# Kernel tuning notes

Hardware: AMD Instinct MI355X
Metric: run time of the kernel (lower is better)

## Reference

```python
import jax, jax.numpy as jnp
import numpy as np

D_IN = 1024
D_OUT = 1024
N_HEADS = 16
HEAD_DIM = D_OUT // N_HEADS


def setup_inputs() -> dict:
    key = jax.random.key(0)
    ks = jax.random.split(key, 5)
    scale = 0.02
    x = jax.random.normal(ks[0], (2, 2048, D_IN), dtype=jnp.float32)
    Wq = jax.random.normal(ks[1], (D_IN, D_OUT), dtype=jnp.float32) * scale
    Wk = jax.random.normal(ks[2], (D_IN, D_OUT), dtype=jnp.float32) * scale
    Wv = jax.random.normal(ks[3], (D_IN, D_OUT), dtype=jnp.float32) * scale
    Wout = jax.random.normal(ks[4], (D_OUT, D_OUT), dtype=jnp.float32) * scale
    return {"x": x, "Wq": Wq, "Wk": Wk, "Wv": Wv, "Wout": Wout}


def reference(x, Wq, Wk, Wv, Wout):
    batch, seq_len, _ = x.shape
    # projections (no bias)
    Q = (x @ Wq).reshape(batch, seq_len, N_HEADS, HEAD_DIM)
    K = (x @ Wk).reshape(batch, seq_len, N_HEADS, HEAD_DIM)
    V = (x @ Wv).reshape(batch, seq_len, N_HEADS, HEAD_DIM)
    # scores: [batch, heads, seq, seq]
    scores = jnp.einsum("bqhd,bkhd->bhqk", Q, K) / jnp.sqrt(
        jnp.asarray(HEAD_DIM, dtype=x.dtype)
    )
    # causal mask: positions k > q masked to -inf
    causal = jnp.tril(jnp.ones((seq_len, seq_len), dtype=bool))
    scores = jnp.where(causal[None, None], scores, -jnp.inf)
    weights = jax.nn.softmax(scores, axis=-1)
    vectors = jnp.einsum("bhqk,bkhd->bqhd", weights, V)
    vectors = vectors.reshape(batch, seq_len, D_OUT)
    return vectors @ Wout
```

## Files before the change

### kernel.cpp

```cpp
#include <hip/hip_runtime.h>
#include <hip/hip_bf16.h>


typedef __attribute__((ext_vector_type(8))) _Float16 vhalf8;
typedef __attribute__((ext_vector_type(4))) _Float16 vhalf4;
typedef __attribute__((ext_vector_type(4))) float vfloat4;

#define D_MODEL 1024
#define SEQ     2048
#define NB      2
#define NH      16
#define HD      64

#define SCALE_K1 0.18033688f

__device__ __forceinline__ void async16(const void* g, void* l) {
  __builtin_amdgcn_global_load_lds(
      (const __attribute__((address_space(1))) unsigned int*)g,
      (__attribute__((address_space(3))) unsigned int*)l, 16, 0, 0);
}

__global__ __launch_bounds__(256) void cvt_f32_f16(
    const float* __restrict__ in, _Float16* __restrict__ out) {
  size_t i = ((size_t)blockIdx.x * 256 + threadIdx.x) * 8;
  float4 a = *(const float4*)&in[i];
  float4 b = *(const float4*)&in[i + 4];
  vhalf8 h;
  h[0] = (_Float16)a.x; h[1] = (_Float16)a.y;
  h[2] = (_Float16)a.z; h[3] = (_Float16)a.w;
  h[4] = (_Float16)b.x; h[5] = (_Float16)b.y;
  h[6] = (_Float16)b.z; h[7] = (_Float16)b.w;
  *(vhalf8*)&out[i] = h;
}

__global__ __launch_bounds__(256) void transpose_w4(
    const float* __restrict__ Wq, const float* __restrict__ Wk,
    const float* __restrict__ Wv, const float* __restrict__ Wo,
    _Float16* __restrict__ Wt_qkv, _Float16* __restrict__ Wot) {
  __shared__ _Float16 tile[64][65];
  int z = blockIdx.z;
  const float* in = (z == 0) ? Wq : (z == 1) ? Wk : (z == 2) ? Wv : Wo;
  _Float16* out = (z < 3) ? (Wt_qkv + (size_t)z * 1024 * 1024) : Wot;
  int c0 = blockIdx.x * 64, r0 = blockIdx.y * 64;
  int t = threadIdx.x;
  int tc = t & 63, tr = t >> 6;
#pragma unroll
  for (int p = 0; p < 16; p++) {
    int r = tr + p * 4;
    tile[r][tc] = (_Float16)in[(size_t)(r0 + r) * 1024 + c0 + tc];
  }
  __syncthreads();
#pragma unroll
  for (int p = 0; p < 16; p++) {
    int r = tr + p * 4;
    out[(size_t)(c0 + r) * 1024 + r0 + tc] = tile[tc][r];
  }
}

__global__ __launch_bounds__(256) void gemm128(
    const _Float16* __restrict__ A, const _Float16* __restrict__ Bt,
    _Float16* __restrict__ Ch, float* __restrict__ Cf,
    _Float16* __restrict__ Vt, int M, int N, int K, int mode) {
  __shared__ _Float16 As[128 * 32];
  __shared__ _Float16 Bs[128 * 32];
  int m0 = blockIdx.x * 128, n0 = blockIdx.y * 128;
  int t = threadIdx.x;
  int lane = t & 63, wave = t >> 6;
  int wm = (wave >> 1) * 64, wn = (wave & 1) * 64;
  int col = lane & 15, quad = lane >> 4;
  int srow = lane >> 2;
  int skc = (lane & 3) << 3;

  vfloat4 acc[4][4];
#pragma unroll
  for (int i = 0; i < 4; i++)
#pragma unroll
    for (int j = 0; j < 4; j++) {
      acc[i][j][0] = 0.f; acc[i][j][1] = 0.f;
      acc[i][j][2] = 0.f; acc[i][j][3] = 0.f;
    }

  for (int k0 = 0; k0 < K; k0 += 32) {
    __syncthreads();
#pragma unroll
    for (int j = 0; j < 4; j++) {
      int c = wave * 4 + j;
      int row = ((c & 7) << 4) + srow;
      if (c < 8)
        async16(&A[(size_t)(m0 + row) * K + k0 + skc], &As[c * 512]);
      else
        async16(&Bt[(size_t)(n0 + row) * K + k0 + skc], &Bs[(c - 8) * 512]);
    }
    __syncthreads();

    vhalf8 af[4], bf[4];
#pragma unroll
    for (int i = 0; i < 4; i++) {
      af[i] = *(const vhalf8*)&As[(wm + i * 16 + col) * 32 + quad * 8];
      bf[i] = *(const vhalf8*)&Bs[(wn + i * 16 + col) * 32 + quad * 8];
    }
#pragma unroll
    for (int i = 0; i < 4; i++)
#pragma unroll
      for (int j = 0; j < 4; j++)
        acc[i][j] = __builtin_amdgcn_mfma_f32_16x16x32_f16(af[i], bf[j], acc[i][j], 0, 0, 0);
  }

  bool vmode = (mode == 2) && (n0 >= 2048);
#pragma unroll
  for (int i = 0; i < 4; i++)
#pragma unroll
    for (int j = 0; j < 4; j++)
#pragma unroll
      for (int r = 0; r < 4; r++) {
        int m = m0 + wm + i * 16 + quad * 4 + r;
        int n = n0 + wn + j * 16 + col;
        if (mode == 1) {
          Cf[(size_t)m * N + n] = acc[i][j][r];
        } else if (vmode) {
          int nn = n - 2048;
          int hh = nn >> 6, dd = nn & 63;
          int bb = m >> 11, ss = m & 2047;
          Vt[(((size_t)bb * NH + hh) * HD + dd) * SEQ + ss] = (_Float16)acc[i][j][r];
        } else {
          Ch[(size_t)m * N + n] = (_Float16)acc[i][j][r];
        }
      }
}

__global__ __launch_bounds__(256) void attn(
    const _Float16* __restrict__ QKV, const _Float16* __restrict__ Vt,
    _Float16* __restrict__ Vec) {
  int blk = blockIdx.x;
  int qt = 31 - (blk >> 5);
  int hb = blk & 31;
  int h = hb & 15;
  int b = hb >> 4;
  int q0 = qt * 64;

  const _Float16* Qb  = QKV + (size_t)(b * SEQ) * 3072 + h * HD;
  const _Float16* Kb  = QKV + (size_t)(b * SEQ) * 3072 + 1024 + h * HD;
  const _Float16* Vtb = Vt + (size_t)(b * NH + h) * HD * SEQ;

  int t = threadIdx.x;
  int lane = t & 63, wave = t >> 6;
  int col = lane & 15, quad = lane >> 4;
  int wq0 = q0 + wave * 16;

  __shared__ _Float16 Ks[64][72];
  __shared__ _Float16 Vs[64][72];
  __shared__ _Float16 Ps[4][16][72];

  vhalf8 qf0 = *(const vhalf8*)&Qb[(size_t)(wq0 + col) * 3072 + quad * 8];
  vhalf8 qf1 = *(const vhalf8*)&Qb[(size_t)(wq0 + col) * 3072 + 32 + quad * 8];
#pragma unroll
  for (int i = 0; i < 8; i++) {
    qf0[i] = qf0[i] * (_Float16)SCALE_K1;
    qf1[i] = qf1[i] * (_Float16)SCALE_K1;
  }

  vfloat4 o[4];
#pragma unroll
  for (int i = 0; i < 4; i++) { o[i][0]=0.f; o[i][1]=0.f; o[i][2]=0.f; o[i][3]=0.f; }
  float lsum[4] = {0.f, 0.f, 0.f, 0.f};

  int srow = t >> 2;
  int scol = (t & 3) * 16;
  int kslot = ((srow & 3) << 4) + (srow >> 2);

  vhalf8 kr0, kr1, vr0, vr1;
  {
    const _Float16* kg = &Kb[(size_t)srow * 3072 + scol];
    kr0 = *(const vhalf8*)kg; kr1 = *(const vhalf8*)(kg + 8);
    const _Float16* vg = &Vtb[(size_t)srow * SEQ + scol];
    vr0 = *(const vhalf8*)vg; vr1 = *(const vhalf8*)(vg + 8);
  }

  for (int kb = 0; kb <= q0 + 63; kb += 64) {
    *(vhalf8*)&Ks[kslot][scol]     = kr0;
    *(vhalf8*)&Ks[kslot][scol + 8] = kr1;
    *(vhalf8*)&Vs[srow][scol]      = vr0;
    *(vhalf8*)&Vs[srow][scol + 8]  = vr1;
    __syncthreads();

    if (kb < q0) {
      const _Float16* kg = &Kb[(size_t)(kb + 64 + srow) * 3072 + scol];
      kr0 = *(const vhalf8*)kg; kr1 = *(const vhalf8*)(kg + 8);
      const _Float16* vg = &Vtb[(size_t)srow * SEQ + kb + 64 + scol];
      vr0 = *(const vhalf8*)vg; vr1 = *(const vhalf8*)(vg + 8);
    }

    if (kb <= wq0 + 15) {
      vfloat4 s[4];
#pragma unroll
      for (int hh = 0; hh < 4; hh++) {
        vhalf8 kf0 = *(const vhalf8*)&Ks[hh * 16 + col][quad * 8];
        vhalf8 kf1 = *(const vhalf8*)&Ks[hh * 16 + col][32 + quad * 8];
        vfloat4 z; z[0]=0.f; z[1]=0.f; z[2]=0.f; z[3]=0.f;
        z = __builtin_amdgcn_mfma_f32_16x16x32_f16(qf0, kf0, z, 0, 0, 0);
        z = __builtin_amdgcn_mfma_f32_16x16x32_f16(qf1, kf1, z, 0, 0, 0);
        s[hh] = z;
      }
      bool diag = (kb + 63 > wq0);
#pragma unroll
      for (int r = 0; r < 4; r++) {
        int q = wq0 + quad * 4 + r;
        float p[4];
#pragma unroll
        for (int hh = 0; hh < 4; hh++) {
          float sc = s[hh][r];
          if (diag && (kb + 4 * col + hh > q)) sc = -1e30f;
          p[hh] = __builtin_exp2f(sc);
        }
        lsum[r] += (p[0] + p[1]) + (p[2] + p[3]);
        vhalf4 ph;
        ph[0] = (_Float16)p[0]; ph[1] = (_Float16)p[1];
        ph[2] = (_Float16)p[2]; ph[3] = (_Float16)p[3];
        *(vhalf4*)&Ps[wave][quad * 4 + r][4 * col] = ph;
      }
      __asm__ __volatile__("s_waitcnt lgkmcnt(0)" ::: "memory");
      vhalf8 pf0 = *(const vhalf8*)&Ps[wave][col][quad * 8];
      vhalf8 pf1 = *(const vhalf8*)&Ps[wave][col][32 + quad * 8];
#pragma unroll
      for (int tt = 0; tt < 4; tt++) {
        vhalf8 vf0 = *(const vhalf8*)&Vs[tt * 16 + col][quad * 8];
        vhalf8 vf1 = *(const vhalf8*)&Vs[tt * 16 + col][32 + quad * 8];
        o[tt] = __builtin_amdgcn_mfma_f32_16x16x32_f16(pf0, vf0, o[tt], 0, 0, 0);
        o[tt] = __builtin_amdgcn_mfma_f32_16x16x32_f16(pf1, vf1, o[tt], 0, 0, 0);
      }
    }
    __syncthreads();
  }

  float inv_l[4];
#pragma unroll
  for (int r = 0; r < 4; r++) {
    float rs = lsum[r];
#pragma unroll
    for (int msk = 1; msk < 16; msk <<= 1) rs += __shfl_xor(rs, msk, 64);
    inv_l[r] = 1.0f / rs;
  }
#pragma unroll
  for (int tt = 0; tt < 4; tt++)
#pragma unroll
    for (int r = 0; r < 4; r++) {
      int q = wq0 + quad * 4 + r;
      int d = tt * 16 + col;
      Vec[(size_t)(b * SEQ + q) * D_MODEL + h * HD + d] =
          (_Float16)(o[tt][r] * inv_l[r]);
    }
}

extern "C" void kernel_launch(void* const* d_in, const int* in_sizes, int n_in,
                              void* d_out, int out_size, void* d_ws, size_t ws_size,
                              hipStream_t stream) {
  const float* x  = (const float*)d_in[0];
  const float* Wq = (const float*)d_in[1];
  const float* Wk = (const float*)d_in[2];
  const float* Wv = (const float*)d_in[3];
  const float* Wo = (const float*)d_in[4];
  float* out = (float*)d_out;

  char* ws = (char*)d_ws;
  _Float16* Xh     = (_Float16*)ws;
  _Float16* Wt_qkv = (_Float16*)(ws + 8388608);
  _Float16* Wot    = (_Float16*)(ws + 14680064);
  _Float16* QKV    = (_Float16*)(ws + 16777216);
  _Float16* Vt     = (_Float16*)(ws + 41943040);
  _Float16* Vec    = (_Float16*)(ws + 50331648);

  dim3 tb(256);
  cvt_f32_f16<<<dim3(2048), tb, 0, stream>>>(x, Xh);
  transpose_w4<<<dim3(16, 16, 4), tb, 0, stream>>>(Wq, Wk, Wv, Wo, Wt_qkv, Wot);

  gemm128<<<dim3(32, 24), tb, 0, stream>>>(Xh, Wt_qkv, QKV, nullptr, Vt,
                                           4096, 3072, 1024, 2);
  attn<<<dim3(NB * NH * (SEQ / 64)), tb, 0, stream>>>(QKV, Vt, Vec);
  gemm128<<<dim3(32, 8), tb, 0, stream>>>(Vec, Wot, nullptr, out, nullptr,
                                          4096, 1024, 1024, 1);
}
```

Baseline: 193.4 us.

## Fuse prep kernels, template GEMM tile width, widen attention blocks, swizzle K smem

Merges the x conversion and weight transpose into one prep launch. Templates the GEMM on N-tile width and uses 64-wide tiles for the output projection so it launches more blocks. The attention kernel now uses 512 threads covering 128 queries per block, sharing each K/V tile across eight waves, and XOR-swizzles the K shared-memory layout to cut bank conflicts. This halves the attention block count and raises per-block work, which may unbalance the causal workload.

```diff
diff --git a/kernel.cpp b/kernel.cpp
--- a/kernel.cpp
+++ b/kernel.cpp
@@ -20,29 +20,34 @@
       (__attribute__((address_space(3))) unsigned int*)l, 16, 0, 0);
 }
 
-__global__ __launch_bounds__(256) void cvt_f32_f16(
-    const float* __restrict__ in, _Float16* __restrict__ out) {
-  size_t i = ((size_t)blockIdx.x * 256 + threadIdx.x) * 8;
-  float4 a = *(const float4*)&in[i];
-  float4 b = *(const float4*)&in[i + 4];
-  vhalf8 h;
-  h[0] = (_Float16)a.x; h[1] = (_Float16)a.y;
-  h[2] = (_Float16)a.z; h[3] = (_Float16)a.w;
-  h[4] = (_Float16)b.x; h[5] = (_Float16)b.y;
-  h[6] = (_Float16)b.z; h[7] = (_Float16)b.w;
-  *(vhalf8*)&out[i] = h;
-}
-
-__global__ __launch_bounds__(256) void transpose_w4(
+__global__ __launch_bounds__(256) void prep(
+    const float* __restrict__ x,
     const float* __restrict__ Wq, const float* __restrict__ Wk,
     const float* __restrict__ Wv, const float* __restrict__ Wo,
-    _Float16* __restrict__ Wt_qkv, _Float16* __restrict__ Wot) {
+    _Float16* __restrict__ Xh, _Float16* __restrict__ Wt_qkv,
+    _Float16* __restrict__ Wot) {
+  int z = blockIdx.z;
+  int t = threadIdx.x;
+  if (z == 4) {
+    int id = blockIdx.y * 16 + blockIdx.x;
+#pragma unroll
+    for (int pass = 0; pass < 8; pass++) {
+      size_t i = ((size_t)(pass * 256 + id) * 256 + t) * 8;
+      float4 a = *(const float4*)&x[i];
+      float4 b = *(const float4*)&x[i + 4];
+      vhalf8 h;
+      h[0] = (_Float16)a.x; h[1] = (_Float16)a.y;
+      h[2] = (_Float16)a.z; h[3] = (_Float16)a.w;
+      h[4] = (_Float16)b.x; h[5] = (_Float16)b.y;
+      h[6] = (_Float16)b.z; h[7] = (_Float16)b.w;
+      *(vhalf8*)&Xh[i] = h;
+    }
+    return;
+  }
   __shared__ _Float16 tile[64][65];
-  int z = blockIdx.z;
   const float* in = (z == 0) ? Wq : (z == 1) ? Wk : (z == 2) ? Wv : Wo;
   _Float16* out = (z < 3) ? (Wt_qkv + (size_t)z * 1024 * 1024) : Wot;
   int c0 = blockIdx.x * 64, r0 = blockIdx.y * 64;
-  int t = threadIdx.x;
   int tc = t & 63, tr = t >> 6;
 #pragma unroll
   for (int p = 0; p < 16; p++) {
@@ -57,25 +62,29 @@
   }
 }
 
+template <int BN>
 __global__ __launch_bounds__(256) void gemm128(
     const _Float16* __restrict__ A, const _Float16* __restrict__ Bt,
     _Float16* __restrict__ Ch, float* __restrict__ Cf,
     _Float16* __restrict__ Vt, int M, int N, int K, int mode) {
+  constexpr int NC = 8 + BN / 16;
+  constexpr int CPW = NC / 4;
+  constexpr int JN = BN / 32;
   __shared__ _Float16 As[128 * 32];
-  __shared__ _Float16 Bs[128 * 32];
-  int m0 = blockIdx.x * 128, n0 = blockIdx.y * 128;
+  __shared__ _Float16 Bs[BN * 32];
+  int m0 = blockIdx.x * 128, n0 = blockIdx.y * BN;
   int t = threadIdx.x;
   int lane = t & 63, wave = t >> 6;
-  int wm = (wave >> 1) * 64, wn = (wave & 1) * 64;
+  int wm = (wave >> 1) * 64, wn = (wave & 1) * (BN / 2);
   int col = lane & 15, quad = lane >> 4;
   int srow = lane >> 2;
   int skc = (lane & 3) << 3;
 
-  vfloat4 acc[4][4];
+  vfloat4 acc[4][JN];
 #pragma unroll
   for (int i = 0; i < 4; i++)
 #pragma unroll
-    for (int j = 0; j < 4; j++) {
+    for (int j = 0; j < JN; j++) {
       acc[i][j][0] = 0.f; acc[i][j][1] = 0.f;
       acc[i][j][2] = 0.f; acc[i][j][3] = 0.f;
     }
@@ -83,9 +92,9 @@
   for (int k0 = 0; k0 < K; k0 += 32) {
     __syncthreads();
 #pragma unroll
-    for (int j = 0; j < 4; j++) {
-      int c = wave * 4 + j;
-      int row = ((c & 7) << 4) + srow;
+    for (int j = 0; j < CPW; j++) {
+      int c = wave * CPW + j;
+      int row = ((c < 8) ? c : (c - 8)) * 16 + srow;
       if (c < 8)
         async16(&A[(size_t)(m0 + row) * K + k0 + skc], &As[c * 512]);
       else
@@ -93,16 +102,17 @@
     }
     __syncthreads();
 
-    vhalf8 af[4], bf[4];
-#pragma unroll
-    for (int i = 0; i < 4; i++) {
+    vhalf8 af[4], bf[JN];
+#pragma unroll
+    for (int i = 0; i < 4; i++)
       af[i] = *(const vhalf8*)&As[(wm + i * 16 + col) * 32 + quad * 8];
-      bf[i] = *(const vhalf8*)&Bs[(wn + i * 16 + col) * 32 + quad * 8];
-    }
+#pragma unroll
+    for (int j = 0; j < JN; j++)
+      bf[j] = *(const vhalf8*)&Bs[(wn + j * 16 + col) * 32 + quad * 8];
 #pragma unroll
     for (int i = 0; i < 4; i++)
 #pragma unroll
-      for (int j = 0; j < 4; j++)
+      for (int j = 0; j < JN; j++)
         acc[i][j] = __builtin_amdgcn_mfma_f32_16x16x32_f16(af[i], bf[j], acc[i][j], 0, 0, 0);
   }
 
@@ -110,7 +120,7 @@
 #pragma unroll
   for (int i = 0; i < 4; i++)
 #pragma unroll
-    for (int j = 0; j < 4; j++)
+    for (int j = 0; j < JN; j++)
 #pragma unroll
       for (int r = 0; r < 4; r++) {
         int m = m0 + wm + i * 16 + quad * 4 + r;
@@ -128,15 +138,15 @@
       }
 }
 
-__global__ __launch_bounds__(256) void attn(
+__global__ __launch_bounds__(512) void attn(
     const _Float16* __restrict__ QKV, const _Float16* __restrict__ Vt,
     _Float16* __restrict__ Vec) {
   int blk = blockIdx.x;
-  int qt = 31 - (blk >> 5);
+  int qt = 15 - (blk >> 5);
   int hb = blk & 31;
   int h = hb & 15;
   int b = hb >> 4;
-  int q0 = qt * 64;
+  int q0 = qt * 128;
 
   const _Float16* Qb  = QKV + (size_t)(b * SEQ) * 3072 + h * HD;
   const _Float16* Kb  = QKV + (size_t)(b * SEQ) * 3072 + 1024 + h * HD;
@@ -149,7 +159,7 @@
 
   __shared__ _Float16 Ks[64][72];
   __shared__ _Float16 Vs[64][72];
-  __shared__ _Float16 Ps[4][16][72];
+  __shared__ _Float16 Ps[8][16][72];
 
   vhalf8 qf0 = *(const vhalf8*)&Qb[(size_t)(wq0 + col) * 3072 + quad * 8];
   vhalf8 qf1 = *(const vhalf8*)&Qb[(size_t)(wq0 + col) * 3072 + 32 + quad * 8];
@@ -164,38 +174,32 @@
   for (int i = 0; i < 4; i++) { o[i][0]=0.f; o[i][1]=0.f; o[i][2]=0.f; o[i][3]=0.f; }
   float lsum[4] = {0.f, 0.f, 0.f, 0.f};
 
-  int srow = t >> 2;
-  int scol = (t & 3) * 16;
+  int srow = t >> 3;
+  int scol = (t & 7) * 8;
   int kslot = ((srow & 3) << 4) + (srow >> 2);
-
-  vhalf8 kr0, kr1, vr0, vr1;
-  {
-    const _Float16* kg = &Kb[(size_t)srow * 3072 + scol];
-    kr0 = *(const vhalf8*)kg; kr1 = *(const vhalf8*)(kg + 8);
-    const _Float16* vg = &Vtb[(size_t)srow * SEQ + scol];
-    vr0 = *(const vhalf8*)vg; vr1 = *(const vhalf8*)(vg + 8);
-  }
-
-  for (int kb = 0; kb <= q0 + 63; kb += 64) {
-    *(vhalf8*)&Ks[kslot][scol]     = kr0;
-    *(vhalf8*)&Ks[kslot][scol + 8] = kr1;
-    *(vhalf8*)&Vs[srow][scol]      = vr0;
-    *(vhalf8*)&Vs[srow][scol + 8]  = vr1;
-    __syncthreads();
-
-    if (kb < q0) {
-      const _Float16* kg = &Kb[(size_t)(kb + 64 + srow) * 3072 + scol];
-      kr0 = *(const vhalf8*)kg; kr1 = *(const vhalf8*)(kg + 8);
-      const _Float16* vg = &Vtb[(size_t)srow * SEQ + kb + 64 + scol];
-      vr0 = *(const vhalf8*)vg; vr1 = *(const vhalf8*)(vg + 8);
+  int kcol = scol ^ ((srow & 3) << 4);
+
+  vhalf8 kr, vr;
+  kr = *(const vhalf8*)&Kb[(size_t)srow * 3072 + scol];
+  vr = *(const vhalf8*)&Vtb[(size_t)srow * SEQ + scol];
+
+  for (int kb = 0; kb <= q0 + 127; kb += 64) {
+    *(vhalf8*)&Ks[kslot][kcol] = kr;
+    *(vhalf8*)&Vs[srow][scol]  = vr;
+    __syncthreads();
+
+    if (kb < q0 + 64) {
+      kr = *(const vhalf8*)&Kb[(size_t)(kb + 64 + srow) * 3072 + scol];
+      vr = *(const vhalf8*)&Vtb[(size_t)srow * SEQ + kb + 64 + scol];
     }
 
     if (kb <= wq0 + 15) {
       vfloat4 s[4];
 #pragma unroll
       for (int hh = 0; hh < 4; hh++) {
-        vhalf8 kf0 = *(const vhalf8*)&Ks[hh * 16 + col][quad * 8];
-        vhalf8 kf1 = *(const vhalf8*)&Ks[hh * 16 + col][32 + quad * 8];
+        int sw = hh << 4;
+        vhalf8 kf0 = *(const vhalf8*)&Ks[hh * 16 + col][(quad * 8) ^ sw];
+        vhalf8 kf1 = *(const vhalf8*)&Ks[hh * 16 + col][(32 + quad * 8) ^ sw];
         vfloat4 z; z[0]=0.f; z[1]=0.f; z[2]=0.f; z[3]=0.f;
         z = __builtin_amdgcn_mfma_f32_16x16x32_f16(qf0, kf0, z, 0, 0, 0);
         z = __builtin_amdgcn_mfma_f32_16x16x32_f16(qf1, kf1, z, 0, 0, 0);
@@ -270,12 +274,10 @@
   _Float16* Vec    = (_Float16*)(ws + 50331648);
 
   dim3 tb(256);
-  cvt_f32_f16<<<dim3(2048), tb, 0, stream>>>(x, Xh);
-  transpose_w4<<<dim3(16, 16, 4), tb, 0, stream>>>(Wq, Wk, Wv, Wo, Wt_qkv, Wot);
-
-  gemm128<<<dim3(32, 24), tb, 0, stream>>>(Xh, Wt_qkv, QKV, nullptr, Vt,
-                                           4096, 3072, 1024, 2);
-  attn<<<dim3(NB * NH * (SEQ / 64)), tb, 0, stream>>>(QKV, Vt, Vec);
-  gemm128<<<dim3(32, 8), tb, 0, stream>>>(Vec, Wot, nullptr, out, nullptr,
-                                          4096, 1024, 1024, 1);
-}
+  prep<<<dim3(16, 16, 5), tb, 0, stream>>>(x, Wq, Wk, Wv, Wo, Xh, Wt_qkv, Wot);
+  gemm128<128><<<dim3(32, 24), tb, 0, stream>>>(Xh, Wt_qkv, QKV, nullptr, Vt,
+                                                4096, 3072, 1024, 2);
+  attn<<<dim3(512), dim3(512), 0, stream>>>(QKV, Vt, Vec);
+  gemm128<64><<<dim3(32, 16), tb, 0, stream>>>(Vec, Wot, nullptr, out, nullptr,
+                                               4096, 1024, 1024, 1);
+}
```

Result: no change. 193.1 us (-0.2%).
